# Performance work log

Hardware: AMD Instinct MI355X
Metric: run time of the kernel (lower is better)

The kernel has to match this reference:

```python
import jax, jax.numpy as jnp
import numpy as np

N = 8192
F_IN = 256
F_OUT = 256
S = 128          # state_dim
D_INNER = 512    # int(2.0 * out_features)


def _ln(x, g, b, eps=1e-5):
    m = x.mean(-1, keepdims=True)
    v = ((x - m) ** 2).mean(-1, keepdims=True)
    return (x - m) / jnp.sqrt(v + eps) * g + b


def setup_inputs() -> dict:
    key = jax.random.key(0)
    ks = jax.random.split(key, 20)
    s = 0.05
    d = {}
    d['h'] = jax.random.normal(ks[0], (N, F_IN), dtype=jnp.float32)
    d['adj'] = jax.random.randint(ks[1], (N, N), 0, 2, dtype=jnp.int32)
    d['W'] = jax.random.normal(ks[2], (F_IN, F_OUT), dtype=jnp.float32) * s
    d['a_src'] = jax.random.normal(ks[3], (F_OUT, 1), dtype=jnp.float32) * s
    d['a_dst'] = jax.random.normal(ks[4], (F_OUT, 1), dtype=jnp.float32) * s
    d['W_bcdt'] = jax.random.normal(ks[5], (F_OUT, 3 * S), dtype=jnp.float32) * s
    d['b_bcdt'] = jnp.zeros((3 * S,), jnp.float32)
    d['abp_w'] = jax.random.normal(ks[6], (S, F_OUT), dtype=jnp.float32) * s
    d['abp_b'] = jnp.zeros((F_OUT,), jnp.float32)
    d['cp_w'] = jax.random.normal(ks[7], (S, 1), dtype=jnp.float32) * s
    d['cp_b'] = jnp.zeros((1,), jnp.float32)
    d['W_hz'] = jax.random.normal(ks[8], (F_OUT, 2 * D_INNER), dtype=jnp.float32) * s
    d['b_hz'] = jnp.zeros((2 * D_INNER,), jnp.float32)
    d['out_w'] = jax.random.normal(ks[9], (D_INNER, F_OUT), dtype=jnp.float32) * s
    d['out_b'] = jnp.zeros((F_OUT,), jnp.float32)
    d['fe1_w'] = jax.random.normal(ks[10], (F_OUT, D_INNER), dtype=jnp.float32) * s
    d['fe1_b'] = jnp.zeros((D_INNER,), jnp.float32)
    d['fe_ln_g'] = jnp.ones((D_INNER,), jnp.float32)
    d['fe_ln_b'] = jnp.zeros((D_INNER,), jnp.float32)
    d['fe2_w'] = jax.random.normal(ks[11], (D_INNER, F_OUT), dtype=jnp.float32) * s
    d['fe2_b'] = jnp.zeros((F_OUT,), jnp.float32)
    d['A'] = jax.random.uniform(ks[12], (S,), minval=1.0, maxval=64.0, dtype=jnp.float32)
    d['D'] = jnp.ones((1,), jnp.float32)
    d['g1_w'] = jax.random.normal(ks[13], (2 * F_OUT, 2 * F_OUT), dtype=jnp.float32) * s
    d['g1_b'] = jnp.zeros((2 * F_OUT,), jnp.float32)
    d['g_ln_g'] = jnp.ones((2 * F_OUT,), jnp.float32)
    d['g_ln_b'] = jnp.zeros((2 * F_OUT,), jnp.float32)
    d['g2_w'] = jax.random.normal(ks[14], (2 * F_OUT, F_OUT), dtype=jnp.float32) * s
    d['g2_b'] = jnp.zeros((F_OUT,), jnp.float32)
    d['ln_g'] = jnp.ones((F_OUT,), jnp.float32)
    d['ln_b'] = jnp.zeros((F_OUT,), jnp.float32)
    return d


def reference(h, adj, W, a_src, a_dst, W_bcdt, b_bcdt, abp_w, abp_b, cp_w, cp_b,
              W_hz, b_hz, out_w, out_b, fe1_w, fe1_b, fe_ln_g, fe_ln_b, fe2_w,
              fe2_b, A, D, g1_w, g1_b, g_ln_g, g_ln_b, g2_w, g2_b, ln_g, ln_b):
    Wh = h @ W                                   # [N, F_OUT]
    # GAT-style masked attention
    e = Wh @ a_src + (Wh @ a_dst).T              # [N, N]
    e = jnp.where(e > 0, e, 0.2 * e)             # leaky_relu(0.2)
    e = jnp.where(adj > 0, e, jnp.float32(-9e15))
    attn = jax.nn.softmax(e, axis=1)
    h_attn = attn @ Wh                           # [N, F_OUT]
    # feature enhancer
    h_enh = jax.nn.silu(_ln(Wh @ fe1_w + fe1_b, fe_ln_g, fe_ln_b)) @ fe2_w + fe2_b
    # SSM-like branch
    BCdt = Wh @ W_bcdt + b_bcdt                  # [N, 3S]
    B, C, dt = jnp.split(BCdt, 3, axis=1)
    Asm = jax.nn.softmax(dt + A[None, :], axis=1)
    ab = (Asm * B) @ abp_w + abp_b               # [N, F_OUT]
    hs = Wh * ab
    hz = hs @ W_hz + b_hz                        # [N, 2*D_INNER]
    h_part, z = jnp.split(hz, 2, axis=1)
    hs = (h_part * jax.nn.silu(z) + h_part * D) @ out_w + out_b
    c_proj = C @ cp_w + cp_b                     # [N, 1]
    hs = hs * (1.0 + c_proj)
    # gated fusion
    comb = jnp.concatenate([h_attn, hs], axis=1)  # [N, 2*F_OUT]
    g = jax.nn.sigmoid(jax.nn.silu(_ln(comb @ g1_w + g1_b, g_ln_g, g_ln_b)) @ g2_w + g2_b)
    fused = g * h_attn + (1.0 - g) * hs + h_enh
    return _ln(fused, ln_g, ln_b)
```

## Files before the change

kernel.cpp:

```cpp
#include <hip/hip_runtime.h>
#include <cstdint>

typedef __attribute__((ext_vector_type(8))) short short8;
typedef __attribute__((ext_vector_type(4))) float f32x4;

#define DEVINL static __device__ __forceinline__

DEVINL ushort f2b(float f) {
    uint32_t u = __builtin_bit_cast(uint32_t, f);
    u += 0x7FFFu + ((u >> 16) & 1u);
    return (ushort)(u >> 16);
}

typedef __attribute__((address_space(3))) uint32_t lds_u32;
typedef const __attribute__((address_space(1))) uint32_t glb_u32;

DEVINL void load_lds_16(const ushort* g, ushort* l) {
    __builtin_amdgcn_global_load_lds((glb_u32*)g, (lds_u32*)l, 16, 0, 0);
}

constexpr int EPI_F32      = 0;
constexpr int EPI_MUL_BF16 = 2;
constexpr int EPI_SCALE_FB = 3;

template<int K, int EPI>
DEVINL void gemm_k_dev(
    const ushort* __restrict__ A, const ushort* __restrict__ BT,
    const float* __restrict__ bias, int N,
    float* __restrict__ outf, ushort* __restrict__ outb, int obld, int oboff,
    const float* __restrict__ extra, int bx, int by,
    ushort* Asm, ushort* Bsm)
{
    const int wave = threadIdx.x >> 6;
    const int lane = threadIdx.x & 63;
    const int quad = lane >> 4, l16 = lane & 15;
    const int lr = lane >> 3, ls = lane & 7;
    const int m0 = bx * 64, n0 = by * 64;

    f32x4 zero = {0.f, 0.f, 0.f, 0.f};
    f32x4 acc[4] = {zero, zero, zero, zero};

    for (int k0 = 0; k0 < K; k0 += 64) {
        #pragma unroll
        for (int p = 0; p < 2; ++p) {
            const int r = wave * 16 + p * 8 + lr;
            load_lds_16(A + (size_t)(m0 + r) * K + k0 + ((ls ^ (r & 7)) * 8),
                        Asm + (size_t)(wave * 16 + p * 8) * 64);
            load_lds_16(BT + (size_t)(n0 + r) * K + k0 + ((ls ^ (r & 7)) * 8),
                        Bsm + (size_t)(wave * 16 + p * 8) * 64);
        }
        __syncthreads();
        #pragma unroll
        for (int ks = 0; ks < 2; ++ks) {
            const int sl = ((ks * 4 + quad) ^ (l16 & 7)) * 8;
            short8 af = *(const short8*)(Asm + (wave * 16 + l16) * 64 + sl);
            #pragma unroll
            for (int c = 0; c < 4; ++c) {
                short8 bf = *(const short8*)(Bsm + (c * 16 + l16) * 64 + sl);
                acc[c] = __builtin_amdgcn_mfma_f32_16x16x32_bf16(af, bf, acc[c], 0, 0, 0);
            }
        }
        __syncthreads();
    }

    #pragma unroll
    for (int r = 0; r < 4; ++r) {
        const int row = m0 + wave * 16 + quad * 4 + r;
        #pragma unroll
        for (int c = 0; c < 4; ++c) {
            const int col = n0 + c * 16 + l16;
            float v = acc[c][r] + (bias ? bias[col] : 0.f);
            if (EPI == EPI_MUL_BF16) v *= extra[(size_t)row * N + col];
            if (EPI == EPI_SCALE_FB) v *= extra[row];
            if (EPI == EPI_F32 || EPI == EPI_SCALE_FB)
                outf[(size_t)row * N + col] = v;
            if (EPI == EPI_MUL_BF16 || EPI == EPI_SCALE_FB)
                outb[(size_t)row * obld + oboff + col] = f2b(v);
        }
    }
}

__global__ __launch_bounds__(256) void gemm_wh_kernel(
    const ushort* __restrict__ A, const ushort* __restrict__ BT,
    const float* __restrict__ asrc, const float* __restrict__ adst,
    float* __restrict__ Wh, ushort* __restrict__ Whbf, ushort* __restrict__ WhT,
    float* __restrict__ sOut, float* __restrict__ dOut)
{
    __shared__ ushort smem[2 * 64 * 64];
    ushort* Asm = smem;
    ushort* Bsm = smem + 4096;
    constexpr int K = 256;

    const int tid = threadIdx.x;
    const int wave = tid >> 6, lane = tid & 63;
    const int quad = lane >> 4, l16 = lane & 15;
    const int lr = lane >> 3, ls = lane & 7;
    const int m0 = blockIdx.x * 64, n0 = blockIdx.y * 64;

    f32x4 zero = {0.f, 0.f, 0.f, 0.f};
    f32x4 acc[4] = {zero, zero, zero, zero};

    for (int k0 = 0; k0 < K; k0 += 64) {
        #pragma unroll
        for (int p = 0; p < 2; ++p) {
            const int r = wave * 16 + p * 8 + lr;
            load_lds_16(A + (size_t)(m0 + r) * K + k0 + ((ls ^ (r & 7)) * 8),
                        Asm + (size_t)(wave * 16 + p * 8) * 64);
            load_lds_16(BT + (size_t)(n0 + r) * K + k0 + ((ls ^ (r & 7)) * 8),
                        Bsm + (size_t)(wave * 16 + p * 8) * 64);
        }
        __syncthreads();
        #pragma unroll
        for (int ks = 0; ks < 2; ++ks) {
            const int sl = ((ks * 4 + quad) ^ (l16 & 7)) * 8;
            short8 af = *(const short8*)(Asm + (wave * 16 + l16) * 64 + sl);
            #pragma unroll
            for (int c = 0; c < 4; ++c) {
                short8 bf = *(const short8*)(Bsm + (c * 16 + l16) * 64 + sl);
                acc[c] = __builtin_amdgcn_mfma_f32_16x16x32_bf16(af, bf, acc[c], 0, 0, 0);
            }
        }
        __syncthreads();
    }

    ushort* Tsm = smem;
    #pragma unroll
    for (int r = 0; r < 4; ++r) {
        const int rl = wave * 16 + quad * 4 + r;
        const int row = m0 + rl;
        float sp = 0.f, dp = 0.f;
        #pragma unroll
        for (int c = 0; c < 4; ++c) {
            const int cl = c * 16 + l16;
            const int col = n0 + cl;
            const float v = acc[c][r];
            Wh[(size_t)row * 256 + col] = v;
            const ushort b = f2b(v);
            Whbf[(size_t)row * 256 + col] = b;
            Tsm[cl * 72 + rl] = b;
            sp += v * asrc[col]; dp += v * adst[col];
        }
        #pragma unroll
        for (int o = 1; o < 16; o <<= 1) {
            sp += __shfl_xor(sp, o);
            dp += __shfl_xor(dp, o);
        }
        if (l16 == 0) {
            atomicAdd(&sOut[row], sp);
            atomicAdd(&dOut[row], dp);
        }
    }
    __syncthreads();
    const int cl = tid >> 2, seg = tid & 3;
    const ushort* src = Tsm + cl * 72 + seg * 16;
    ushort* dst = WhT + (size_t)(n0 + cl) * 8192 + m0 + seg * 16;
    *(uint4*)(dst)     = *(const uint4*)(src);
    *(uint4*)(dst + 8) = *(const uint4*)(src + 8);
}

constexpr int EPR_LNSILU = 0;
constexpr int EPR_BCDT   = 1;
constexpr int EPR_HZ     = 2;
constexpr int EPR_FINAL  = 3;

template<int K, int N, int EPI>
DEVINL void gemm_row_dev(
    const ushort* __restrict__ A, const ushort* __restrict__ BT,
    const float* __restrict__ bias,
    float* __restrict__ outf, ushort* __restrict__ outb,
    const float* __restrict__ q0, const float* __restrict__ q1,
    const float* __restrict__ q2, const float* __restrict__ q3,
    const float* __restrict__ q4,
    int bx, int by, ushort* Asm, ushort* Bsm, float* red)
{
    constexpr int NW = N / 4;
    constexpr int NF = NW / 16;

    const int wave = threadIdx.x >> 6;
    const int lane = threadIdx.x & 63;
    const int quad = lane >> 4, l16 = lane & 15;
    const int lr = lane >> 3, ls = lane & 7;
    const int m0 = bx * 16;
    const ushort* Bb = BT + (EPI == EPR_HZ ? (size_t)by * 512 * K : 0);

    f32x4 zero = {0.f, 0.f, 0.f, 0.f};
    f32x4 acc[NF];
    #pragma unroll
    for (int c = 0; c < NF; ++c) acc[c] = zero;

    for (int k0 = 0; k0 < K; k0 += 64) {
        if (wave < 2) {
            const int r = wave * 8 + lr;
            load_lds_16(A + (size_t)(m0 + r) * K + k0 + ((ls ^ (r & 7)) * 8),
                        Asm + (size_t)(wave * 8) * 64);
        }
        #pragma unroll
        for (int p = 0; p < NW / 8; ++p) {
            const int n = wave * NW + p * 8 + lr;
            load_lds_16(Bb + (size_t)n * K + k0 + ((ls ^ (n & 7)) * 8),
                        Bsm + (size_t)(wave * NW + p * 8) * 64);
        }
        __syncthreads();
        #pragma unroll
        for (int ks = 0; ks < 2; ++ks) {
            const int sl = ((ks * 4 + quad) ^ (l16 & 7)) * 8;
            short8 af = *(const short8*)(Asm + l16 * 64 + sl);
            #pragma unroll
            for (int c = 0; c < NF; ++c) {
                const int gf = (EPI == EPR_BCDT) ? (wave + 4 * c) : (wave * NF + c);
                short8 bf = *(const short8*)(Bsm + (gf * 16 + l16) * 64 + sl);
                acc[c] = __builtin_amdgcn_mfma_f32_16x16x32_bf16(af, bf, acc[c], 0, 0, 0);
            }
        }
        __syncthreads();
    }

    if constexpr (EPI != EPR_HZ) {
        #pragma unroll
        for (int c = 0; c < NF; ++c) {
            const int gf = (EPI == EPR_BCDT) ? (wave + 4 * c) : (wave * NF + c);
            const float bs = bias[gf * 16 + l16];
            #pragma unroll
            for (int r = 0; r < 4; ++r) acc[c][r] += bs;
        }
    }

    if constexpr (EPI == EPR_LNSILU) {
        float s[4], q[4];
        #pragma unroll
        for (int r = 0; r < 4; ++r) {
            s[r] = 0.f; q[r] = 0.f;
            #pragma unroll
            for (int c = 0; c < NF; ++c) { const float v = acc[c][r]; s[r] += v; q[r] += v * v; }
            #pragma unroll
            for (int o = 1; o < 16; o <<= 1) { s[r] += __shfl_xor(s[r], o); q[r] += __shfl_xor(q[r], o); }
        }
        if (l16 == 0) {
            #pragma unroll
            for (int r = 0; r < 4; ++r) {
                red[(quad * 4 + r) * 8 + wave * 2]     = s[r];
                red[(quad * 4 + r) * 8 + wave * 2 + 1] = q[r];
            }
        }
        __syncthreads();
        #pragma unroll
        for (int r = 0; r < 4; ++r) {
            const int row16 = quad * 4 + r;
            float S = 0.f, Q = 0.f;
            #pragma unroll
            for (int w = 0; w < 4; ++w) { S += red[row16 * 8 + w * 2]; Q += red[row16 * 8 + w * 2 + 1]; }
            const float mean = S * (1.f / N);
            const float rstd = rsqrtf(Q * (1.f / N) - mean * mean + 1e-5f);
            #pragma unroll
            for (int c = 0; c < NF; ++c) {
                const int col = (wave * NF + c) * 16 + l16;
                const float y = (acc[c][r] - mean) * rstd * q0[col] + q1[col];
                outb[(size_t)(m0 + row16) * N + col] = f2b(y / (1.f + __expf(-y)));
            }
        }
    } else if constexpr (EPI == EPR_BCDT) {
        float t[2][4], e[2][4];
        #pragma unroll
        for (int ci = 0; ci < 2; ++ci) {
            const int dcol = (wave + 4 * (ci + 4)) * 16 - 256 + l16;
            const float av = q0[dcol];
            #pragma unroll
            for (int r = 0; r < 4; ++r) t[ci][r] = acc[ci + 4][r] + av;
        }
        float pm[4];
        #pragma unroll
        for (int r = 0; r < 4; ++r) {
            pm[r] = fmaxf(t[0][r], t[1][r]);
            #pragma unroll
            for (int o = 1; o < 16; o <<= 1) pm[r] = fmaxf(pm[r], __shfl_xor(pm[r], o));
        }
        if (l16 == 0) {
            #pragma unroll
            for (int r = 0; r < 4; ++r) red[(quad * 4 + r) * 4 + wave] = pm[r];
        }
        __syncthreads();
        float mx[4];
        #pragma unroll
        for (int r = 0; r < 4; ++r) {
            const int row16 = quad * 4 + r;
            mx[r] = fmaxf(fmaxf(red[row16 * 4], red[row16 * 4 + 1]),
                          fmaxf(red[row16 * 4 + 2], red[row16 * 4 + 3]));
        }
        float pe[4], pc[4];
        #pragma unroll
        for (int r = 0; r < 4; ++r) {
            e[0][r] = __expf(t[0][r] - mx[r]);
            e[1][r] = __expf(t[1][r] - mx[r]);
            pe[r] = e[0][r] + e[1][r];
            pc[r] = 0.f;
            #pragma unroll
            for (int ci = 0; ci < 2; ++ci) {
                const int ccol = (wave + 4 * (ci + 2)) * 16 - 128 + l16;
                pc[r] += acc[ci + 2][r] * q1[ccol];
            }
            #pragma unroll
            for (int o = 1; o < 16; o <<= 1) { pe[r] += __shfl_xor(pe[r], o); pc[r] += __shfl_xor(pc[r], o); }
        }
        if (l16 == 0) {
            #pragma unroll
            for (int r = 0; r < 4; ++r) {
                red[64  + (quad * 4 + r) * 4 + wave] = pe[r];
                red[128 + (quad * 4 + r) * 4 + wave] = pc[r];
            }
        }
        __syncthreads();
        #pragma unroll
        for (int r = 0; r < 4; ++r) {
            const int row16 = quad * 4 + r;
            const float inv = 1.f / (red[64 + row16 * 4] + red[64 + row16 * 4 + 1] +
                                     red[64 + row16 * 4 + 2] + red[64 + row16 * 4 + 3]);
            #pragma unroll
            for (int ci = 0; ci < 2; ++ci) {
                const int bcol = (wave + 4 * ci) * 16 + l16;
                outb[(size_t)(m0 + row16) * 128 + bcol] = f2b(acc[ci][r] * e[ci][r] * inv);
            }
        }
        if (wave == 0 && l16 == 0) {
            #pragma unroll
            for (int r = 0; r < 4; ++r) {
                const int row16 = quad * 4 + r;
                outf[m0 + row16] = 1.f + red[128 + row16 * 4] + red[128 + row16 * 4 + 1] +
                                   red[128 + row16 * 4 + 2] + red[128 + row16 * 4 + 3] + q2[0];
            }
        }
    } else if constexpr (EPI == EPR_HZ) {
        float* ep = (float*)Bsm;
        const float D0 = q0[0];
        if (wave >= 2) {
            #pragma unroll
            for (int c = 0; c < NF; ++c) {
                const int lc = (wave * NF + c) * 16 + l16;
                const float bz = bias[512 + by * 256 + lc - 256];
                #pragma unroll
                for (int r = 0; r < 4; ++r) {
                    const float z = acc[c][r] + bz;
                    ep[(quad * 4 + r) * 256 + lc - 256] = z / (1.f + __expf(-z)) + D0;
                }
            }
        }
        __syncthreads();
        if (wave < 2) {
            #pragma unroll
            for (int c = 0; c < NF; ++c) {
                const int lc = (wave * NF + c) * 16 + l16;
                const float bh = bias[by * 256 + lc];
                #pragma unroll
                for (int r = 0; r < 4; ++r) {
                    const float v = (acc[c][r] + bh) * ep[(quad * 4 + r) * 256 + lc];
                    outb[(size_t)(m0 + quad * 4 + r) * 512 + by * 256 + lc] = f2b(v);
                }
            }
        }
    } else {
        float fv[NF][4], s[4], q[4];
        #pragma unroll
        for (int r = 0; r < 4; ++r) { s[r] = 0.f; q[r] = 0.f; }
        #pragma unroll
        for (int c = 0; c < NF; ++c) {
            const int col = (wave * NF + c) * 16 + l16;
            #pragma unroll
            for (int r = 0; r < 4; ++r) {
                const size_t idx = (size_t)(m0 + quad * 4 + r) * 256 + col;
                const float g = 1.f / (1.f + __expf(-acc[c][r]));
                const float f = g * q0[idx] + (1.f - g) * q1[idx] + q2[idx];
                fv[c][r] = f; s[r] += f; q[r] += f * f;
            }
        }
        #pragma unroll
        for (int r = 0; r < 4; ++r) {
            #pragma unroll
            for (int o = 1; o < 16; o <<= 1) { s[r] += __shfl_xor(s[r], o); q[r] += __shfl_xor(q[r], o); }
        }
        if (l16 == 0) {
            #pragma unroll
            for (int r = 0; r < 4; ++r) {
                red[(quad * 4 + r) * 8 + wave * 2]     = s[r];
                red[(quad * 4 + r) * 8 + wave * 2 + 1] = q[r];
            }
        }
        __syncthreads();
        #pragma unroll
        for (int r = 0; r < 4; ++r) {
            const int row16 = quad * 4 + r;
            float S = 0.f, Q = 0.f;
            #pragma unroll
            for (int w = 0; w < 4; ++w) { S += red[row16 * 8 + w * 2]; Q += red[row16 * 8 + w * 2 + 1]; }
            const float mean = S * (1.f / 256.f);
            const float rstd = rsqrtf(Q * (1.f / 256.f) - mean * mean + 1e-5f);
            #pragma unroll
            for (int c = 0; c < NF; ++c) {
                const int col = (wave * NF + c) * 16 + l16;
                outf[(size_t)(m0 + row16) * 256 + col] = (fv[c][r] - mean) * rstd * q3[col] + q4[col];
            }
        }
    }
}

__global__ __launch_bounds__(256, 3) void attn_kernel(
    const int* __restrict__ adj, const float* __restrict__ sA,
    const float* __restrict__ dA, const ushort* __restrict__ WhT,
    float* __restrict__ Upart, float* __restrict__ lpart)
{
    __shared__ ushort vsm[256 * 64];
    __shared__ ushort wsm[64 * 64];

    const int tid  = threadIdx.x;
    const int wave = tid >> 6, lane = tid & 63, quad = lane >> 4, l16 = lane & 15;
    const int lr = lane >> 3, ls = lane & 7;
    const int i0 = blockIdx.x * 64;
    const int js = blockIdx.y;
    const int jbase = js * 1024;
    const int pr = tid >> 2, pc = tid & 3;
    const float s_r = sA[i0 + pr];
    const int* adjp = adj + (size_t)(i0 + pr) * 8192 + jbase;
    const int rt = wave & 1, ch = wave >> 1;

    f32x4 zero = {0.f, 0.f, 0.f, 0.f};
    f32x4 acc[2][8] = {{zero, zero, zero, zero, zero, zero, zero, zero},
                       {zero, zero, zero, zero, zero, zero, zero, zero}};
    float lsum = 0.f;

    int4 ca[2][2];
    #pragma unroll
    for (int gi = 0; gi < 2; ++gi) {
        const int g = pc + gi * 4;
        ca[gi][0] = *(const int4*)(adjp + g * 8);
        ca[gi][1] = *(const int4*)(adjp + g * 8 + 4);
    }

    for (int c64 = 0; c64 < 1024; c64 += 64) {
        #pragma unroll
        for (int p = 0; p < 8; ++p) {
            const int f = wave * 64 + p * 8 + lr;
            load_lds_16(WhT + (size_t)f * 8192 + jbase + c64 + ((ls ^ (f & 7)) * 8),
                        vsm + (size_t)(wave * 64 + p * 8) * 64);
        }
        const bool more = (c64 + 64 < 1024);
        int4 na[2][2];
        if (more) {
            #pragma unroll
            for (int gi = 0; gi < 2; ++gi) {
                const int g = pc + gi * 4;
                na[gi][0] = *(const int4*)(adjp + c64 + 64 + g * 8);
                na[gi][1] = *(const int4*)(adjp + c64 + 64 + g * 8 + 4);
            }
        }
        #pragma unroll
        for (int gi = 0; gi < 2; ++gi) {
            const int g = pc + gi * 4;
            const float4 d0 = *(const float4*)(dA + jbase + c64 + g * 8);
            const float4 d1 = *(const float4*)(dA + jbase + c64 + g * 8 + 4);
            const int   aa[8] = {ca[gi][0].x, ca[gi][0].y, ca[gi][0].z, ca[gi][0].w,
                                 ca[gi][1].x, ca[gi][1].y, ca[gi][1].z, ca[gi][1].w};
            const float dd[8] = {d0.x, d0.y, d0.z, d0.w, d1.x, d1.y, d1.z, d1.w};
            union { ushort us[8]; uint4 v; } pk;
            #pragma unroll
            for (int q = 0; q < 8; ++q) {
                float e = s_r + dd[q];
                e = fmaxf(e, 0.2f * e);
                const float w = aa[q] ? __expf(e) : 0.f;
                lsum += w; pk.us[q] = f2b(w);
            }
            *(uint4*)(wsm + pr * 64 + ((g ^ (pr & 7)) * 8)) = pk.v;
        }
        __syncthreads();

        #pragma unroll
        for (int ks = 0; ks < 2; ++ks) {
            const int sl = ((ks * 4 + quad) ^ (l16 & 7)) * 8;
            short8 a0 = *(const short8*)(wsm + (rt * 32 + l16) * 64 + sl);
            short8 a1 = *(const short8*)(wsm + (rt * 32 + 16 + l16) * 64 + sl);
            #pragma unroll
            for (int c = 0; c < 8; ++c) {
                short8 bf = *(const short8*)(vsm + (ch * 128 + c * 16 + l16) * 64 + sl);
                acc[0][c] = __builtin_amdgcn_mfma_f32_16x16x32_bf16(a0, bf, acc[0][c], 0, 0, 0);
                acc[1][c] = __builtin_amdgcn_mfma_f32_16x16x32_bf16(a1, bf, acc[1][c], 0, 0, 0);
            }
        }
        __syncthreads();
        if (more) {
            #pragma unroll
            for (int gi = 0; gi < 2; ++gi) {
                ca[gi][0] = na[gi][0];
                ca[gi][1] = na[gi][1];
            }
        }
    }

    lsum += __shfl_down(lsum, 1);
    lsum += __shfl_down(lsum, 2);
    if (pc == 0) lpart[(size_t)js * 8192 + i0 + pr] = lsum;

    #pragma unroll
    for (int it = 0; it < 2; ++it) {
        #pragma unroll
        for (int c = 0; c < 8; ++c) {
            const int col = ch * 128 + c * 16 + l16;
            #pragma unroll
            for (int r = 0; r < 4; ++r) {
                const int row = i0 + rt * 32 + it * 16 + quad * 4 + r;
                Upart[((size_t)js * 8192 + row) * 256 + col] = acc[it][c][r];
            }
        }
    }
}

__global__ __launch_bounds__(256) void post_attn_kernel(
    const float* __restrict__ Upart, const float* __restrict__ lpart,
    float* __restrict__ hattn, ushort* __restrict__ comb,
    const ushort* __restrict__ Whbf,
    const ushort* __restrict__ fe1T, const float* __restrict__ fe1_b,
    const float* __restrict__ fe_ln_g, const float* __restrict__ fe_ln_b,
    ushort* __restrict__ tact,
    const ushort* __restrict__ bcdtT, const float* __restrict__ b_bcdt,
    const float* __restrict__ Avec, const float* __restrict__ cpw,
    const float* __restrict__ cpb,
    ushort* __restrict__ SB, float* __restrict__ cscl)
{
    __shared__ ushort Asm[16 * 64];
    __shared__ ushort Bsm[512 * 64];
    __shared__ float red[192];
    const int b = blockIdx.x;

    if (b < 2048) {
        const int row = b * 4 + (threadIdx.x >> 6);
        const int lane = threadIdx.x & 63;
        float l = 0.f;
        #pragma unroll
        for (int js = 0; js < 8; ++js) l += lpart[(size_t)js * 8192 + row];
        const float inv = 1.f / l;
        float4 u = {0.f, 0.f, 0.f, 0.f};
        #pragma unroll
        for (int js = 0; js < 8; ++js) {
            const float4 t = *(const float4*)&Upart[((size_t)js * 8192 + row) * 256 + lane * 4];
            u.x += t.x; u.y += t.y; u.z += t.z; u.w += t.w;
        }
        u.x *= inv; u.y *= inv; u.z *= inv; u.w *= inv;
        *(float4*)&hattn[(size_t)row * 256 + lane * 4] = u;
        union { ushort us[4]; uint2 v; } pk;
        pk.us[0] = f2b(u.x); pk.us[1] = f2b(u.y); pk.us[2] = f2b(u.z); pk.us[3] = f2b(u.w);
        *(uint2*)&comb[(size_t)row * 512 + lane * 4] = pk.v;
    } else if (b < 2560) {
        gemm_row_dev<256, 512, EPR_LNSILU>(Whbf, fe1T, fe1_b, nullptr, tact,
            fe_ln_g, fe_ln_b, nullptr, nullptr, nullptr, b - 2048, 0, Asm, Bsm, red);
    } else {
        gemm_row_dev<256, 384, EPR_BCDT>(Whbf, bcdtT, b_bcdt, cscl, SB,
            Avec, cpw, cpb, nullptr, nullptr, b - 2560, 0, Asm, Bsm, red);
    }
}

__global__ __launch_bounds__(256) void gemm_fe2_sb_kernel(
    const ushort* __restrict__ tact, const ushort* __restrict__ fe2T,
    const float* __restrict__ fe2_b, float* __restrict__ henh,
    const ushort* __restrict__ SB, const ushort* __restrict__ abpT,
    const float* __restrict__ abp_b, ushort* __restrict__ hsbf,
    const float* __restrict__ Wh)
{
    __shared__ ushort Asm[64 * 64];
    __shared__ ushort Bsm[64 * 64];
    const int b = blockIdx.x;
    if (b < 512)
        gemm_k_dev<512, EPI_F32>(tact, fe2T, fe2_b, 256, henh, nullptr, 0, 0,
                                 nullptr, b & 127, b >> 7, Asm, Bsm);
    else
        gemm_k_dev<128, EPI_MUL_BF16>(SB, abpT, abp_b, 256, nullptr, hsbf, 256, 0,
                                      Wh, (b - 512) & 127, (b - 512) >> 7, Asm, Bsm);
}

__global__ __launch_bounds__(256) void gemm_hz_kernel(
    const ushort* __restrict__ hsbf, const ushort* __restrict__ hzT,
    const float* __restrict__ b_hz, ushort* __restrict__ vbf,
    const float* __restrict__ Dvec)
{
    __shared__ ushort Asm[16 * 64];
    __shared__ ushort Bsm[512 * 64];
    __shared__ float red[192];
    gemm_row_dev<256, 512, EPR_HZ>(hsbf, hzT, b_hz, nullptr, vbf, Dvec,
        nullptr, nullptr, nullptr, nullptr, blockIdx.x, blockIdx.y, Asm, Bsm, red);
}

__global__ __launch_bounds__(256) void gemm_out_kernel(
    const ushort* __restrict__ vbf, const ushort* __restrict__ outT,
    const float* __restrict__ out_b, float* __restrict__ hs2,
    ushort* __restrict__ comb, const float* __restrict__ cscl)
{
    __shared__ ushort Asm[64 * 64];
    __shared__ ushort Bsm[64 * 64];
    gemm_k_dev<512, EPI_SCALE_FB>(vbf, outT, out_b, 256, hs2, comb, 512, 256,
                                  cscl, blockIdx.x, blockIdx.y, Asm, Bsm);
}

__global__ __launch_bounds__(256) void gemm_g1_kernel(
    const ushort* __restrict__ comb, const ushort* __restrict__ g1T,
    const float* __restrict__ g1_b, ushort* __restrict__ tact,
    const float* __restrict__ g_ln_g, const float* __restrict__ g_ln_b)
{
    __shared__ ushort Asm[16 * 64];
    __shared__ ushort Bsm[512 * 64];
    __shared__ float red[192];
    gemm_row_dev<512, 512, EPR_LNSILU>(comb, g1T, g1_b, nullptr, tact,
        g_ln_g, g_ln_b, nullptr, nullptr, nullptr, blockIdx.x, 0, Asm, Bsm, red);
}

__global__ __launch_bounds__(256) void gemm_final_kernel(
    const ushort* __restrict__ tact, const ushort* __restrict__ g2T,
    const float* __restrict__ g2_b, float* __restrict__ outp,
    const float* __restrict__ hattn, const float* __restrict__ hs2,
    const float* __restrict__ henh, const float* __restrict__ ln_g,
    const float* __restrict__ ln_b)
{
    __shared__ ushort Asm[16 * 64];
    __shared__ ushort Bsm[256 * 64];
    __shared__ float red[192];
    gemm_row_dev<512, 256, EPR_FINAL>(tact, g2T, g2_b, outp, nullptr,
        hattn, hs2, henh, ln_g, ln_b, blockIdx.x, 0, Asm, Bsm, red);
}

struct TJob { const float* in; ushort* out; int R, C, off, perm; };
struct TArgs { TJob j[10]; };

DEVINL int hzperm(int j) {
    return (j < 512) ? ((j >> 8) << 9) + (j & 255)
                     : (((j - 512) >> 8) << 9) + 256 + ((j - 512) & 255);
}

__global__ __launch_bounds__(256) void multi_transpose_kernel(TArgs a)
{
    __shared__ float tile[32][33];
    const int b = blockIdx.x;
    int ji = 0;
    #pragma unroll
    for (int k = 1; k < 10; ++k) if (b >= a.j[k].off) ji = k;
    const TJob J = a.j[ji];
    const int t = b - J.off;

    if (J.R == 0) {
        const int base = t * 1024 + threadIdx.x;
        #pragma unroll
        for (int k = 0; k < 4; ++k)
            J.out[base + k * 256] = f2b(J.in[base + k * 256]);
        return;
    }
    const int CB = J.C >> 5;
    const int bx = t % CB, by = t / CB;
    const int tx = threadIdx.x & 31, ty = threadIdx.x >> 5;
    const int c0 = bx * 32, r0 = by * 32;
    #pragma unroll
    for (int i = ty; i < 32; i += 8)
        tile[i][tx] = J.in[(size_t)(r0 + i) * J.C + (c0 + tx)];
    __syncthreads();
    #pragma unroll
    for (int i = ty; i < 32; i += 8) {
        int orow = c0 + i;
        if (J.perm) orow = hzperm(orow);
        J.out[(size_t)orow * J.R + (r0 + tx)] = f2b(tile[tx][i]);
    }
}

extern "C" void kernel_launch(void* const* d_in, const int* in_sizes, int n_in,
                              void* d_out, int out_size, void* d_ws, size_t ws_size,
                              hipStream_t stream)
{
    const float* h      = (const float*)d_in[0];
    const int*   adj    = (const int*)  d_in[1];
    const float* W      = (const float*)d_in[2];
    const float* a_src  = (const float*)d_in[3];
    const float* a_dst  = (const float*)d_in[4];
    const float* W_bcdt = (const float*)d_in[5];
    const float* b_bcdt = (const float*)d_in[6];
    const float* abp_w  = (const float*)d_in[7];
    const float* abp_b  = (const float*)d_in[8];
    const float* cp_w   = (const float*)d_in[9];
    const float* cp_b   = (const float*)d_in[10];
    const float* W_hz   = (const float*)d_in[11];
    const float* b_hz   = (const float*)d_in[12];
    const float* out_w  = (const float*)d_in[13];
    const float* out_b  = (const float*)d_in[14];
    const float* fe1_w  = (const float*)d_in[15];
    const float* fe1_b  = (const float*)d_in[16];
    const float* fe_ln_g= (const float*)d_in[17];
    const float* fe_ln_b= (const float*)d_in[18];
    const float* fe2_w  = (const float*)d_in[19];
    const float* fe2_b  = (const float*)d_in[20];
    const float* Avec   = (const float*)d_in[21];
    const float* Dvec   = (const float*)d_in[22];
    const float* g1_w   = (const float*)d_in[23];
    const float* g1_b   = (const float*)d_in[24];
    const float* g_ln_g = (const float*)d_in[25];
    const float* g_ln_b = (const float*)d_in[26];
    const float* g2_w   = (const float*)d_in[27];
    const float* g2_b   = (const float*)d_in[28];
    const float* ln_g   = (const float*)d_in[29];
    const float* ln_b   = (const float*)d_in[30];
    float* outp = (float*)d_out;

    char* p = (char*)d_ws;
    size_t off = 0;
    auto take = [&](size_t nbytes) -> void* {
        void* r = p + off;
        off += (nbytes + 255) & ~(size_t)255;
        return r;
    };
    ushort* wT    = (ushort*)take(256 * 256 * 2);
    ushort* fe1T  = (ushort*)take(512 * 256 * 2);
    ushort* fe2T  = (ushort*)take(256 * 512 * 2);
    ushort* bcdtT = (ushort*)take(384 * 256 * 2);
    ushort* hzT   = (ushort*)take(1024 * 256 * 2);
    ushort* outT  = (ushort*)take(256 * 512 * 2);
    ushort* g1T   = (ushort*)take(512 * 512 * 2);
    ushort* g2T   = (ushort*)take(256 * 512 * 2);
    ushort* abpT  = (ushort*)take(256 * 128 * 2);
    ushort* hbf   = (ushort*)take((size_t)8192 * 256 * 2);
    float*  Wh    = (float*) take((size_t)8192 * 256 * 4);
    ushort* Whbf  = (ushort*)take((size_t)8192 * 256 * 2);
    ushort* WhT   = (ushort*)take((size_t)8192 * 256 * 2);
    float*  sbuf  = (float*) take(8192 * 4);
    float*  dbuf  = (float*) take(8192 * 4);
    float*  cscl  = (float*) take(8192 * 4);
    float*  hattn = (float*) take((size_t)8192 * 256 * 4);
    float*  henh  = (float*) take((size_t)8192 * 256 * 4);
    float*  lpart = (float*) take(8 * 8192 * 4);
    ushort* SB    = (ushort*)take((size_t)8192 * 128 * 2);
    ushort* hsbf  = (ushort*)take((size_t)8192 * 256 * 2);
    ushort* vbf   = (ushort*)take((size_t)8192 * 512 * 2);
    float*  hs2   = (float*) take((size_t)8192 * 256 * 4);
    ushort* comb  = (ushort*)take((size_t)8192 * 512 * 2);
    ushort* tact  = (ushort*)take((size_t)8192 * 512 * 2);
    float*  Upart = (float*) take((size_t)8 * 8192 * 256 * 4);

    (void)in_sizes; (void)n_in; (void)out_size; (void)ws_size;

    hipMemsetAsync(sbuf, 0, 2 * 8192 * sizeof(float), stream);

    {
        TArgs ta; int boff = 0;
        auto addT = [&](int i, const float* in, ushort* out, int R, int C, int perm) {
            ta.j[i] = TJob{in, out, R, C, boff, perm};
            boff += (R / 32) * (C / 32);
        };
        addT(0, W,      wT,    256, 256,  0);
        addT(1, fe1_w,  fe1T,  256, 512,  0);
        addT(2, fe2_w,  fe2T,  512, 256,  0);
        addT(3, W_bcdt, bcdtT, 256, 384,  0);
        addT(4, abp_w,  abpT,  128, 256,  0);
        addT(5, W_hz,   hzT,   256, 1024, 1);
        addT(6, out_w,  outT,  512, 256,  0);
        addT(7, g1_w,   g1T,   512, 512,  0);
        addT(8, g2_w,   g2T,   512, 256,  0);
        ta.j[9] = TJob{h, hbf, 0, 8192 * 256, boff, 0};
        boff += (8192 * 256) / 1024;
        multi_transpose_kernel<<<boff, 256, 0, stream>>>(ta);
    }

    gemm_wh_kernel<<<dim3(128, 4), 256, 0, stream>>>(
        hbf, wT, a_src, a_dst, Wh, Whbf, WhT, sbuf, dbuf);

    attn_kernel<<<dim3(128, 8), 256, 0, stream>>>(adj, sbuf, dbuf, WhT, Upart, lpart);

    post_attn_kernel<<<3072, 256, 0, stream>>>(
        Upart, lpart, hattn, comb, Whbf,
        fe1T, fe1_b, fe_ln_g, fe_ln_b, tact,
        bcdtT, b_bcdt, Avec, cp_w, cp_b, SB, cscl);

    gemm_fe2_sb_kernel<<<1024, 256, 0, stream>>>(
        tact, fe2T, fe2_b, henh, SB, abpT, abp_b, hsbf, Wh);

    gemm_hz_kernel<<<dim3(512, 2), 256, 0, stream>>>(hsbf, hzT, b_hz, vbf, Dvec);

    gemm_out_kernel<<<dim3(128, 4), 256, 0, stream>>>(vbf, outT, out_b, hs2, comb, cscl);

    gemm_g1_kernel<<<512, 256, 0, stream>>>(comb, g1T, g1_b, tact, g_ln_g, g_ln_b);

    gemm_final_kernel<<<512, 256, 0, stream>>>(
        tact, g2T, g2_b, outp, hattn, hs2, henh, ln_g, ln_b);
}
```

Baseline: 620.2 us.

## Double-buffer attention LDS tiles and halve column split count

The attention kernel now uses double-buffered LDS for the Wh tile and the softmax weight tile. It issues the next tile's DMA and adj/dA prefetch, then computes the next weights while MFMAs run on the current buffer, synchronising with custom waitcnt barriers. Each block also covers 2048 columns instead of 1024, so the grid drops from 8 to 4 column splits, and the partial-sum buffers and reductions shrink to match. The aim is to hide global-load latency and cut partial-reduction traffic. The cost is more LDS per block (occupancy bound lowered to 2) and fewer blocks overall, which may leave some CUs idle.

```diff
diff --git a/kernel.cpp b/kernel.cpp
--- a/kernel.cpp
+++ b/kernel.cpp
@@ -18,6 +18,9 @@
 DEVINL void load_lds_16(const ushort* g, ushort* l) {
     __builtin_amdgcn_global_load_lds((glb_u32*)g, (lds_u32*)l, 16, 0, 0);
 }
+
+DEVINL void barrier_vm16() { asm volatile("s_waitcnt vmcnt(16) lgkmcnt(0)\ns_barrier" ::: "memory"); }
+DEVINL void barrier_lgkm() { asm volatile("s_waitcnt lgkmcnt(0)\ns_barrier" ::: "memory"); }
 
 constexpr int EPI_F32      = 0;
 constexpr int EPI_MUL_BF16 = 2;
@@ -286,26 +289,26 @@
             mx[r] = fmaxf(fmaxf(red[row16 * 4], red[row16 * 4 + 1]),
                           fmaxf(red[row16 * 4 + 2], red[row16 * 4 + 3]));
         }
-        float pe[4], pc[4];
+        float pe[4], pc2[4];
         #pragma unroll
         for (int r = 0; r < 4; ++r) {
             e[0][r] = __expf(t[0][r] - mx[r]);
             e[1][r] = __expf(t[1][r] - mx[r]);
             pe[r] = e[0][r] + e[1][r];
-            pc[r] = 0.f;
+            pc2[r] = 0.f;
             #pragma unroll
             for (int ci = 0; ci < 2; ++ci) {
                 const int ccol = (wave + 4 * (ci + 2)) * 16 - 128 + l16;
-                pc[r] += acc[ci + 2][r] * q1[ccol];
-            }
-            #pragma unroll
-            for (int o = 1; o < 16; o <<= 1) { pe[r] += __shfl_xor(pe[r], o); pc[r] += __shfl_xor(pc[r], o); }
+                pc2[r] += acc[ci + 2][r] * q1[ccol];
+            }
+            #pragma unroll
+            for (int o = 1; o < 16; o <<= 1) { pe[r] += __shfl_xor(pe[r], o); pc2[r] += __shfl_xor(pc2[r], o); }
         }
         if (l16 == 0) {
             #pragma unroll
             for (int r = 0; r < 4; ++r) {
                 red[64  + (quad * 4 + r) * 4 + wave] = pe[r];
-                red[128 + (quad * 4 + r) * 4 + wave] = pc[r];
+                red[128 + (quad * 4 + r) * 4 + wave] = pc2[r];
             }
         }
         __syncthreads();
@@ -401,23 +404,95 @@
     }
 }
 
-__global__ __launch_bounds__(256, 3) void attn_kernel(
+#define ATTN_PREF(paN, pdN, T)                                                    \
+    {                                                                              \
+        _Pragma("unroll")                                                          \
+        for (int gi = 0; gi < 2; ++gi) {                                           \
+            const int g = pc + gi * 4;                                             \
+            paN[gi][0] = *(const int4*)(adjp + (T) * 64 + g * 8);                  \
+            paN[gi][1] = *(const int4*)(adjp + (T) * 64 + g * 8 + 4);              \
+            pdN[gi][0] = *(const float4*)(dAp + (T) * 64 + g * 8);                 \
+            pdN[gi][1] = *(const float4*)(dAp + (T) * 64 + g * 8 + 4);             \
+        }                                                                          \
+    }
+
+#define ATTN_DMA(BUF, T)                                                          \
+    {                                                                              \
+        _Pragma("unroll")                                                          \
+        for (int p = 0; p < 8; ++p) {                                              \
+            const int f = wave * 64 + p * 8 + lr;                                  \
+            load_lds_16(WhT + (size_t)f * 8192 + jbase + (T) * 64 + ((ls ^ (f & 7)) * 8), \
+                        vsm[BUF] + (wave * 64 + p * 8) * 64);                      \
+        }                                                                          \
+    }
+
+#define ATTN_PCOMP(paC, pdC, BUF)                                                 \
+    {                                                                              \
+        _Pragma("unroll")                                                          \
+        for (int gi = 0; gi < 2; ++gi) {                                           \
+            const int g = pc + gi * 4;                                             \
+            const int aa[8] = {paC[gi][0].x, paC[gi][0].y, paC[gi][0].z, paC[gi][0].w, \
+                               paC[gi][1].x, paC[gi][1].y, paC[gi][1].z, paC[gi][1].w}; \
+            const float dd[8] = {pdC[gi][0].x, pdC[gi][0].y, pdC[gi][0].z, pdC[gi][0].w, \
+                                 pdC[gi][1].x, pdC[gi][1].y, pdC[gi][1].z, pdC[gi][1].w}; \
+            union { ushort us[8]; uint4 v; } pk;                                   \
+            _Pragma("unroll")                                                      \
+            for (int q = 0; q < 8; ++q) {                                          \
+                float e = s_r + dd[q];                                             \
+                e = fmaxf(e, 0.2f * e);                                            \
+                const float w = aa[q] ? __expf(e) : 0.f;                           \
+                lsum += w; pk.us[q] = f2b(w);                                      \
+            }                                                                      \
+            *(uint4*)(wsm[BUF] + pr * 64 + ((g ^ (pr & 7)) * 8)) = pk.v;           \
+        }                                                                          \
+    }
+
+#define ATTN_MFMA(BUF)                                                            \
+    {                                                                              \
+        _Pragma("unroll")                                                          \
+        for (int ks = 0; ks < 2; ++ks) {                                           \
+            const int sl = ((ks * 4 + quad) ^ (l16 & 7)) * 8;                      \
+            short8 a0 = *(const short8*)(wsm[BUF] + (rt * 32 + l16) * 64 + sl);    \
+            short8 a1 = *(const short8*)(wsm[BUF] + (rt * 32 + 16 + l16) * 64 + sl); \
+            _Pragma("unroll")                                                      \
+            for (int c = 0; c < 8; ++c) {                                          \
+                short8 bf = *(const short8*)(vsm[BUF] + (ch * 128 + c * 16 + l16) * 64 + sl); \
+                acc[0][c] = __builtin_amdgcn_mfma_f32_16x16x32_bf16(a0, bf, acc[0][c], 0, 0, 0); \
+                acc[1][c] = __builtin_amdgcn_mfma_f32_16x16x32_bf16(a1, bf, acc[1][c], 0, 0, 0); \
+            }                                                                      \
+        }                                                                          \
+    }
+
+#define ATTN_ITER(K, MB, PB, paC, pdC, paN, pdN)                                  \
+    {                                                                              \
+        const int tD = ((K) + 1 < 32) ? (K) + 1 : 31;                              \
+        const int tP = ((K) + 2 < 32) ? (K) + 2 : 31;                              \
+        ATTN_DMA(PB, tD)                                                           \
+        ATTN_PREF(paN, pdN, tP)                                                    \
+        if ((K) + 1 < 32) { ATTN_PCOMP(paC, pdC, PB) }                             \
+        barrier_vm16();                                                            \
+        ATTN_MFMA(MB)                                                              \
+        barrier_lgkm();                                                            \
+    }
+
+__global__ __launch_bounds__(256, 2) void attn_kernel(
     const int* __restrict__ adj, const float* __restrict__ sA,
     const float* __restrict__ dA, const ushort* __restrict__ WhT,
     float* __restrict__ Upart, float* __restrict__ lpart)
 {
-    __shared__ ushort vsm[256 * 64];
-    __shared__ ushort wsm[64 * 64];
+    __shared__ ushort vsm[2][256 * 64];
+    __shared__ ushort wsm[2][64 * 64];
 
     const int tid  = threadIdx.x;
     const int wave = tid >> 6, lane = tid & 63, quad = lane >> 4, l16 = lane & 15;
     const int lr = lane >> 3, ls = lane & 7;
     const int i0 = blockIdx.x * 64;
     const int js = blockIdx.y;
-    const int jbase = js * 1024;
+    const int jbase = js * 2048;
     const int pr = tid >> 2, pc = tid & 3;
     const float s_r = sA[i0 + pr];
     const int* adjp = adj + (size_t)(i0 + pr) * 8192 + jbase;
+    const float* dAp = dA + jbase;
     const int rt = wave & 1, ch = wave >> 1;
 
     f32x4 zero = {0.f, 0.f, 0.f, 0.f};
@@ -425,71 +500,18 @@
                        {zero, zero, zero, zero, zero, zero, zero, zero}};
     float lsum = 0.f;
 
-    int4 ca[2][2];
-    #pragma unroll
-    for (int gi = 0; gi < 2; ++gi) {
-        const int g = pc + gi * 4;
-        ca[gi][0] = *(const int4*)(adjp + g * 8);
-        ca[gi][1] = *(const int4*)(adjp + g * 8 + 4);
-    }
-
-    for (int c64 = 0; c64 < 1024; c64 += 64) {
-        #pragma unroll
-        for (int p = 0; p < 8; ++p) {
-            const int f = wave * 64 + p * 8 + lr;
-            load_lds_16(WhT + (size_t)f * 8192 + jbase + c64 + ((ls ^ (f & 7)) * 8),
-                        vsm + (size_t)(wave * 64 + p * 8) * 64);
-        }
-        const bool more = (c64 + 64 < 1024);
-        int4 na[2][2];
-        if (more) {
-            #pragma unroll
-            for (int gi = 0; gi < 2; ++gi) {
-                const int g = pc + gi * 4;
-                na[gi][0] = *(const int4*)(adjp + c64 + 64 + g * 8);
-                na[gi][1] = *(const int4*)(adjp + c64 + 64 + g * 8 + 4);
-            }
-        }
-        #pragma unroll
-        for (int gi = 0; gi < 2; ++gi) {
-            const int g = pc + gi * 4;
-            const float4 d0 = *(const float4*)(dA + jbase + c64 + g * 8);
-            const float4 d1 = *(const float4*)(dA + jbase + c64 + g * 8 + 4);
-            const int   aa[8] = {ca[gi][0].x, ca[gi][0].y, ca[gi][0].z, ca[gi][0].w,
-                                 ca[gi][1].x, ca[gi][1].y, ca[gi][1].z, ca[gi][1].w};
-            const float dd[8] = {d0.x, d0.y, d0.z, d0.w, d1.x, d1.y, d1.z, d1.w};
-            union { ushort us[8]; uint4 v; } pk;
-            #pragma unroll
-            for (int q = 0; q < 8; ++q) {
-                float e = s_r + dd[q];
-                e = fmaxf(e, 0.2f * e);
-                const float w = aa[q] ? __expf(e) : 0.f;
-                lsum += w; pk.us[q] = f2b(w);
-            }
-            *(uint4*)(wsm + pr * 64 + ((g ^ (pr & 7)) * 8)) = pk.v;
-        }
-        __syncthreads();
-
-        #pragma unroll
-        for (int ks = 0; ks < 2; ++ks) {
-            const int sl = ((ks * 4 + quad) ^ (l16 & 7)) * 8;
-            short8 a0 = *(const short8*)(wsm + (rt * 32 + l16) * 64 + sl);
-            short8 a1 = *(const short8*)(wsm + (rt * 32 + 16 + l16) * 64 + sl);
-            #pragma unroll
-            for (int c = 0; c < 8; ++c) {
-                short8 bf = *(const short8*)(vsm + (ch * 128 + c * 16 + l16) * 64 + sl);
-                acc[0][c] = __builtin_amdgcn_mfma_f32_16x16x32_bf16(a0, bf, acc[0][c], 0, 0, 0);
-                acc[1][c] = __builtin_amdgcn_mfma_f32_16x16x32_bf16(a1, bf, acc[1][c], 0, 0, 0);
-            }
-        }
-        __syncthreads();
-        if (more) {
-            #pragma unroll
-            for (int gi = 0; gi < 2; ++gi) {
-                ca[gi][0] = na[gi][0];
-                ca[gi][1] = na[gi][1];
-            }
-        }
+    int4   pa0[2][2], pa1[2][2];
+    float4 pd0[2][2], pd1[2][2];
+
+    ATTN_PREF(pa0, pd0, 0)
+    ATTN_DMA(0, 0)
+    ATTN_PREF(pa1, pd1, 1)
+    ATTN_PCOMP(pa0, pd0, 0)
+
+    #pragma unroll 1
+    for (int k = 0; k < 32; k += 2) {
+        ATTN_ITER(k,     0, 1, pa1, pd1, pa0, pd0)
+        ATTN_ITER(k + 1, 1, 0, pa0, pd0, pa1, pd1)
     }
 
     lsum += __shfl_down(lsum, 1);
@@ -532,11 +554,11 @@
         const int lane = threadIdx.x & 63;
         float l = 0.f;
         #pragma unroll
-        for (int js = 0; js < 8; ++js) l += lpart[(size_t)js * 8192 + row];
+        for (int js = 0; js < 4; ++js) l += lpart[(size_t)js * 8192 + row];
         const float inv = 1.f / l;
         float4 u = {0.f, 0.f, 0.f, 0.f};
         #pragma unroll
-        for (int js = 0; js < 8; ++js) {
+        for (int js = 0; js < 4; ++js) {
             const float4 t = *(const float4*)&Upart[((size_t)js * 8192 + row) * 256 + lane * 4];
             u.x += t.x; u.y += t.y; u.z += t.z; u.w += t.w;
         }
@@ -724,14 +746,14 @@
     float*  cscl  = (float*) take(8192 * 4);
     float*  hattn = (float*) take((size_t)8192 * 256 * 4);
     float*  henh  = (float*) take((size_t)8192 * 256 * 4);
-    float*  lpart = (float*) take(8 * 8192 * 4);
+    float*  lpart = (float*) take(4 * 8192 * 4);
     ushort* SB    = (ushort*)take((size_t)8192 * 128 * 2);
     ushort* hsbf  = (ushort*)take((size_t)8192 * 256 * 2);
     ushort* vbf   = (ushort*)take((size_t)8192 * 512 * 2);
     float*  hs2   = (float*) take((size_t)8192 * 256 * 4);
     ushort* comb  = (ushort*)take((size_t)8192 * 512 * 2);
     ushort* tact  = (ushort*)take((size_t)8192 * 512 * 2);
-    float*  Upart = (float*) take((size_t)8 * 8192 * 256 * 4);
+    float*  Upart = (float*) take((size_t)4 * 8192 * 256 * 4);
 
     (void)in_sizes; (void)n_in; (void)out_size; (void)ws_size;
 
@@ -760,7 +782,7 @@
     gemm_wh_kernel<<<dim3(128, 4), 256, 0, stream>>>(
         hbf, wT, a_src, a_dst, Wh, Whbf, WhT, sbuf, dbuf);
 
-    attn_kernel<<<dim3(128, 8), 256, 0, stream>>>(adj, sbuf, dbuf, WhT, Upart, lpart);
+    attn_kernel<<<dim3(128, 4), 256, 0, stream>>>(adj, sbuf, dbuf, WhT, Upart, lpart);
 
     post_attn_kernel<<<3072, 256, 0, stream>>>(
         Upart, lpart, hattn, comb, Whbf,
```

After: 608.9 us. Within noise of the previous version (-1.8%).

## Store Wh in MFMA fragment layout and drop LDS staging in attention

Applied to the files above, without the earlier changes.

The Wh GEMM now writes the bf16 transposed copy of Wh in an MFMA-B-fragment-ready layout, so the attention kernel can load B operands directly from global memory without LDS staging or block barriers. The attention weights are built per lane in registers and rearranged into A fragments with ds_bpermute instead of going through shared memory. The j-split drops from 8 to 4, which halves the Upart partial buffers and the post-attention reduction but gives fewer blocks and longer per-block loops. This trades LDS traffic and syncs for uncoalesced-risk global fragment loads that rely on L2 reuse and lower grid parallelism.

```diff
diff --git a/kernel.cpp b/kernel.cpp
--- a/kernel.cpp
+++ b/kernel.cpp
@@ -83,7 +83,7 @@
 __global__ __launch_bounds__(256) void gemm_wh_kernel(
     const ushort* __restrict__ A, const ushort* __restrict__ BT,
     const float* __restrict__ asrc, const float* __restrict__ adst,
-    float* __restrict__ Wh, ushort* __restrict__ Whbf, ushort* __restrict__ WhT,
+    float* __restrict__ Wh, ushort* __restrict__ Whbf, ushort* __restrict__ WhF,
     float* __restrict__ sOut, float* __restrict__ dOut)
 {
     __shared__ ushort smem[2 * 64 * 64];
@@ -151,11 +151,12 @@
         }
     }
     __syncthreads();
-    const int cl = tid >> 2, seg = tid & 3;
-    const ushort* src = Tsm + cl * 72 + seg * 16;
-    ushort* dst = WhT + (size_t)(n0 + cl) * 8192 + m0 + seg * 16;
-    *(uint4*)(dst)     = *(const uint4*)(src);
-    *(uint4*)(dst + 8) = *(const uint4*)(src + 8);
+    const int jb0 = m0 >> 5, fb0 = n0 >> 4;
+    #pragma unroll
+    for (int jbl = 0; jbl < 2; ++jbl) {
+        uint4 v = *(const uint4*)(Tsm + (wave * 16 + l16) * 72 + jbl * 32 + quad * 8);
+        *(uint4*)(WhF + ((size_t)((jb0 + jbl) * 16 + fb0 + wave) * 64 + lane) * 8) = v;
+    }
 }
 
 constexpr int EPR_LNSILU = 0;
@@ -286,26 +287,26 @@
             mx[r] = fmaxf(fmaxf(red[row16 * 4], red[row16 * 4 + 1]),
                           fmaxf(red[row16 * 4 + 2], red[row16 * 4 + 3]));
         }
-        float pe[4], pc[4];
+        float pe[4], pc2[4];
         #pragma unroll
         for (int r = 0; r < 4; ++r) {
             e[0][r] = __expf(t[0][r] - mx[r]);
             e[1][r] = __expf(t[1][r] - mx[r]);
             pe[r] = e[0][r] + e[1][r];
-            pc[r] = 0.f;
+            pc2[r] = 0.f;
             #pragma unroll
             for (int ci = 0; ci < 2; ++ci) {
                 const int ccol = (wave + 4 * (ci + 2)) * 16 - 128 + l16;
-                pc[r] += acc[ci + 2][r] * q1[ccol];
-            }
-            #pragma unroll
-            for (int o = 1; o < 16; o <<= 1) { pe[r] += __shfl_xor(pe[r], o); pc[r] += __shfl_xor(pc[r], o); }
+                pc2[r] += acc[ci + 2][r] * q1[ccol];
+            }
+            #pragma unroll
+            for (int o = 1; o < 16; o <<= 1) { pe[r] += __shfl_xor(pe[r], o); pc2[r] += __shfl_xor(pc2[r], o); }
         }
         if (l16 == 0) {
             #pragma unroll
             for (int r = 0; r < 4; ++r) {
                 red[64  + (quad * 4 + r) * 4 + wave] = pe[r];
-                red[128 + (quad * 4 + r) * 4 + wave] = pc[r];
+                red[128 + (quad * 4 + r) * 4 + wave] = pc2[r];
             }
         }
         __syncthreads();
@@ -401,100 +402,79 @@
     }
 }
 
-__global__ __launch_bounds__(256, 3) void attn_kernel(
+__global__ __launch_bounds__(256) void attn_kernel(
     const int* __restrict__ adj, const float* __restrict__ sA,
-    const float* __restrict__ dA, const ushort* __restrict__ WhT,
+    const float* __restrict__ dA, const ushort* __restrict__ WhF,
     float* __restrict__ Upart, float* __restrict__ lpart)
 {
-    __shared__ ushort vsm[256 * 64];
-    __shared__ ushort wsm[64 * 64];
-
     const int tid  = threadIdx.x;
     const int wave = tid >> 6, lane = tid & 63, quad = lane >> 4, l16 = lane & 15;
-    const int lr = lane >> 3, ls = lane & 7;
     const int i0 = blockIdx.x * 64;
     const int js = blockIdx.y;
-    const int jbase = js * 1024;
-    const int pr = tid >> 2, pc = tid & 3;
-    const float s_r = sA[i0 + pr];
-    const int* adjp = adj + (size_t)(i0 + pr) * 8192 + jbase;
+    const int jbase = js * 2048;
+    const int jb0 = jbase >> 5;
     const int rt = wave & 1, ch = wave >> 1;
+    const int rr = lane >> 2, jg = lane & 3;
+    const int row0 = i0 + rt * 32 + rr;
+    const int row1 = row0 + 16;
+    const float s0 = sA[row0], s1 = sA[row1];
+    const int* adj0 = adj + (size_t)row0 * 8192 + jbase + jg * 8;
+    const int* adj1 = adj + (size_t)row1 * 8192 + jbase + jg * 8;
+    const float* dAp = dA + jbase + jg * 8;
+    const int perm = ((l16 << 2) | quad) << 2;
 
     f32x4 zero = {0.f, 0.f, 0.f, 0.f};
     f32x4 acc[2][8] = {{zero, zero, zero, zero, zero, zero, zero, zero},
                        {zero, zero, zero, zero, zero, zero, zero, zero}};
-    float lsum = 0.f;
-
-    int4 ca[2][2];
-    #pragma unroll
-    for (int gi = 0; gi < 2; ++gi) {
-        const int g = pc + gi * 4;
-        ca[gi][0] = *(const int4*)(adjp + g * 8);
-        ca[gi][1] = *(const int4*)(adjp + g * 8 + 4);
-    }
-
-    for (int c64 = 0; c64 < 1024; c64 += 64) {
-        #pragma unroll
-        for (int p = 0; p < 8; ++p) {
-            const int f = wave * 64 + p * 8 + lr;
-            load_lds_16(WhT + (size_t)f * 8192 + jbase + c64 + ((ls ^ (f & 7)) * 8),
-                        vsm + (size_t)(wave * 64 + p * 8) * 64);
-        }
-        const bool more = (c64 + 64 < 1024);
-        int4 na[2][2];
-        if (more) {
-            #pragma unroll
-            for (int gi = 0; gi < 2; ++gi) {
-                const int g = pc + gi * 4;
-                na[gi][0] = *(const int4*)(adjp + c64 + 64 + g * 8);
-                na[gi][1] = *(const int4*)(adjp + c64 + 64 + g * 8 + 4);
-            }
-        }
-        #pragma unroll
-        for (int gi = 0; gi < 2; ++gi) {
-            const int g = pc + gi * 4;
-            const float4 d0 = *(const float4*)(dA + jbase + c64 + g * 8);
-            const float4 d1 = *(const float4*)(dA + jbase + c64 + g * 8 + 4);
-            const int   aa[8] = {ca[gi][0].x, ca[gi][0].y, ca[gi][0].z, ca[gi][0].w,
-                                 ca[gi][1].x, ca[gi][1].y, ca[gi][1].z, ca[gi][1].w};
-            const float dd[8] = {d0.x, d0.y, d0.z, d0.w, d1.x, d1.y, d1.z, d1.w};
-            union { ushort us[8]; uint4 v; } pk;
-            #pragma unroll
-            for (int q = 0; q < 8; ++q) {
-                float e = s_r + dd[q];
-                e = fmaxf(e, 0.2f * e);
-                const float w = aa[q] ? __expf(e) : 0.f;
-                lsum += w; pk.us[q] = f2b(w);
-            }
-            *(uint4*)(wsm + pr * 64 + ((g ^ (pr & 7)) * 8)) = pk.v;
-        }
-        __syncthreads();
-
-        #pragma unroll
-        for (int ks = 0; ks < 2; ++ks) {
-            const int sl = ((ks * 4 + quad) ^ (l16 & 7)) * 8;
-            short8 a0 = *(const short8*)(wsm + (rt * 32 + l16) * 64 + sl);
-            short8 a1 = *(const short8*)(wsm + (rt * 32 + 16 + l16) * 64 + sl);
-            #pragma unroll
-            for (int c = 0; c < 8; ++c) {
-                short8 bf = *(const short8*)(vsm + (ch * 128 + c * 16 + l16) * 64 + sl);
-                acc[0][c] = __builtin_amdgcn_mfma_f32_16x16x32_bf16(a0, bf, acc[0][c], 0, 0, 0);
-                acc[1][c] = __builtin_amdgcn_mfma_f32_16x16x32_bf16(a1, bf, acc[1][c], 0, 0, 0);
-            }
-        }
-        __syncthreads();
-        if (more) {
-            #pragma unroll
-            for (int gi = 0; gi < 2; ++gi) {
-                ca[gi][0] = na[gi][0];
-                ca[gi][1] = na[gi][1];
-            }
-        }
-    }
-
-    lsum += __shfl_down(lsum, 1);
-    lsum += __shfl_down(lsum, 2);
-    if (pc == 0) lpart[(size_t)js * 8192 + i0 + pr] = lsum;
+    float ls0 = 0.f, ls1 = 0.f;
+
+    #pragma unroll 2
+    for (int cb = 0; cb < 64; ++cb) {
+        const int off = cb * 32;
+        const float4 d0 = *(const float4*)(dAp + off);
+        const float4 d1 = *(const float4*)(dAp + off + 4);
+        const int4 a00 = *(const int4*)(adj0 + off);
+        const int4 a01 = *(const int4*)(adj0 + off + 4);
+        const int4 a10 = *(const int4*)(adj1 + off);
+        const int4 a11 = *(const int4*)(adj1 + off + 4);
+        const float dd[8] = {d0.x, d0.y, d0.z, d0.w, d1.x, d1.y, d1.z, d1.w};
+        const int aa0[8] = {a00.x, a00.y, a00.z, a00.w, a01.x, a01.y, a01.z, a01.w};
+        const int aa1[8] = {a10.x, a10.y, a10.z, a10.w, a11.x, a11.y, a11.z, a11.w};
+        ushort us0[8], us1[8];
+        #pragma unroll
+        for (int q = 0; q < 8; ++q) {
+            float e0 = s0 + dd[q];
+            e0 = fmaxf(e0, 0.2f * e0);
+            const float w0 = aa0[q] ? __expf(e0) : 0.f;
+            ls0 += w0; us0[q] = f2b(w0);
+            float e1 = s1 + dd[q];
+            e1 = fmaxf(e1, 0.2f * e1);
+            const float w1 = aa1[q] ? __expf(e1) : 0.f;
+            ls1 += w1; us1[q] = f2b(w1);
+        }
+        union FR { int d[4]; short8 v; } f0, f1;
+        #pragma unroll
+        for (int d = 0; d < 4; ++d) {
+            const int p0 = (int)((uint)us0[2 * d] | ((uint)us0[2 * d + 1] << 16));
+            const int p1 = (int)((uint)us1[2 * d] | ((uint)us1[2 * d + 1] << 16));
+            f0.d[d] = __builtin_amdgcn_ds_bpermute(perm, p0);
+            f1.d[d] = __builtin_amdgcn_ds_bpermute(perm, p1);
+        }
+        const ushort* Bp = WhF + ((size_t)((jb0 + cb) * 16 + ch * 8) * 64 + lane) * 8;
+        #pragma unroll
+        for (int c = 0; c < 8; ++c) {
+            short8 bf = *(const short8*)(Bp + (size_t)c * 64 * 8);
+            acc[0][c] = __builtin_amdgcn_mfma_f32_16x16x32_bf16(f0.v, bf, acc[0][c], 0, 0, 0);
+            acc[1][c] = __builtin_amdgcn_mfma_f32_16x16x32_bf16(f1.v, bf, acc[1][c], 0, 0, 0);
+        }
+    }
+
+    ls0 += __shfl_down(ls0, 1); ls0 += __shfl_down(ls0, 2);
+    ls1 += __shfl_down(ls1, 1); ls1 += __shfl_down(ls1, 2);
+    if (ch == 0 && jg == 0) {
+        lpart[(size_t)js * 8192 + row0] = ls0;
+        lpart[(size_t)js * 8192 + row1] = ls1;
+    }
 
     #pragma unroll
     for (int it = 0; it < 2; ++it) {
@@ -532,11 +512,11 @@
         const int lane = threadIdx.x & 63;
         float l = 0.f;
         #pragma unroll
-        for (int js = 0; js < 8; ++js) l += lpart[(size_t)js * 8192 + row];
+        for (int js = 0; js < 4; ++js) l += lpart[(size_t)js * 8192 + row];
         const float inv = 1.f / l;
         float4 u = {0.f, 0.f, 0.f, 0.f};
         #pragma unroll
-        for (int js = 0; js < 8; ++js) {
+        for (int js = 0; js < 4; ++js) {
             const float4 t = *(const float4*)&Upart[((size_t)js * 8192 + row) * 256 + lane * 4];
             u.x += t.x; u.y += t.y; u.z += t.z; u.w += t.w;
         }
@@ -718,20 +698,20 @@
     ushort* hbf   = (ushort*)take((size_t)8192 * 256 * 2);
     float*  Wh    = (float*) take((size_t)8192 * 256 * 4);
     ushort* Whbf  = (ushort*)take((size_t)8192 * 256 * 2);
-    ushort* WhT   = (ushort*)take((size_t)8192 * 256 * 2);
+    ushort* WhF   = (ushort*)take((size_t)8192 * 256 * 2);
     float*  sbuf  = (float*) take(8192 * 4);
     float*  dbuf  = (float*) take(8192 * 4);
     float*  cscl  = (float*) take(8192 * 4);
     float*  hattn = (float*) take((size_t)8192 * 256 * 4);
     float*  henh  = (float*) take((size_t)8192 * 256 * 4);
-    float*  lpart = (float*) take(8 * 8192 * 4);
+    float*  lpart = (float*) take(4 * 8192 * 4);
     ushort* SB    = (ushort*)take((size_t)8192 * 128 * 2);
     ushort* hsbf  = (ushort*)take((size_t)8192 * 256 * 2);
     ushort* vbf   = (ushort*)take((size_t)8192 * 512 * 2);
     float*  hs2   = (float*) take((size_t)8192 * 256 * 4);
     ushort* comb  = (ushort*)take((size_t)8192 * 512 * 2);
     ushort* tact  = (ushort*)take((size_t)8192 * 512 * 2);
-    float*  Upart = (float*) take((size_t)8 * 8192 * 256 * 4);
+    float*  Upart = (float*) take((size_t)4 * 8192 * 256 * 4);
 
     (void)in_sizes; (void)n_in; (void)out_size; (void)ws_size;
 
@@ -758,9 +738,9 @@
     }
 
     gemm_wh_kernel<<<dim3(128, 4), 256, 0, stream>>>(
-        hbf, wT, a_src, a_dst, Wh, Whbf, WhT, sbuf, dbuf);
-
-    attn_kernel<<<dim3(128, 8), 256, 0, stream>>>(adj, sbuf, dbuf, WhT, Upart, lpart);
+        hbf, wT, a_src, a_dst, Wh, Whbf, WhF, sbuf, dbuf);
+
+    attn_kernel<<<dim3(128, 4), 256, 0, stream>>>(adj, sbuf, dbuf, WhF, Upart, lpart);
 
     post_attn_kernel<<<3072, 256, 0, stream>>>(
         Upart, lpart, hattn, comb, Whbf,
```

Result: no change. 614.5 us (-0.9%).
